# Performance work log

Measured on AMD Instinct MI355X. Metric: run time of the kernel, lower is better.

Reference implementation:

```python
import jax, jax.numpy as jnp
import numpy as np

EPS = 1e-12  # tf.math.l2_normalize epsilon

def l2norm(x):
    # tf.math.l2_normalize: x * rsqrt(max(sum(x^2), eps)) along last axis
    sq = jnp.sum(x * x, axis=-1, keepdims=True)
    return x * jax.lax.rsqrt(jnp.maximum(sq, EPS))

def setup_inputs() -> dict:
    key = jax.random.key(0)
    ks = jax.random.split(key, 10)
    B, L, D = 2, 512, 256
    OD = 256
    return {
        "queries": jax.random.normal(ks[0], (B, L, D), jnp.float32),
        "keys": jax.random.normal(ks[1], (B, L, D), jnp.float32),
        "values": jax.random.normal(ks[2], (B, L, D), jnp.float32),
        "relative_encoding_lookup": jax.random.normal(ks[3], (B, L, L, OD), jnp.float32),
        "edge_type_embedding": jax.random.normal(ks[4], (B, L, L, OD), jnp.float32),
        "Wq": jax.random.normal(ks[5], (D, OD), jnp.float32) * 0.05,
        "bq": jnp.zeros((OD,), jnp.float32),
        "Wk": jax.random.normal(ks[6], (D, OD), jnp.float32) * 0.05,
        "bk": jnp.zeros((OD,), jnp.float32),
        "Wv": jax.random.normal(ks[7], (D, OD), jnp.float32) * 0.05,
        "bv": jnp.zeros((OD,), jnp.float32),
    }

def reference(queries, keys, values, relative_encoding_lookup, edge_type_embedding,
              Wq, bq, Wk, bk, Wv, bv):
    d = queries.shape[-1]  # NOTE: original uses the INPUT dim (pre-projection) for scaling
    q = l2norm(jnp.matmul(queries, Wq) + bq)   # [B,L,OD]
    k = l2norm(jnp.matmul(keys, Wk) + bk)      # [B,L,OD]
    v = l2norm(jnp.matmul(values, Wv) + bv)    # [B,L,OD]
    scores_qk = jnp.einsum('bld,bmd->blm', q, k) * 0.4
    # Original broadcasts q to [B,L,L,OD] then multiply+reduce; expressed here as a
    # batched contraction (same math, no [B,L,L,OD] query broadcast materialized).
    # NOTE: the original computes scores_position (*0.2) but then overwrites it:
    #   scores = scores_ + scores_position; scores = scores_ + scores_edge_embedding
    # so scores_position is dead code and does NOT affect the output.
    scores_edge = jnp.einsum('bld,blmd->blm', q, edge_type_embedding) * 0.6
    inv_sqrt_d = jax.lax.rsqrt(jnp.float32(d))
    scores = (scores_qk + scores_edge) * inv_sqrt_d
    return scores, v, q
```

## Files before the change

kernel.cpp:

```cpp
#include <hip/hip_runtime.h>

#define SEQ_L 512
#define DIM 256

typedef float f4 __attribute__((ext_vector_type(4)));

__global__ __launch_bounds__(256) void proj_norm3_kernel(
    const float* __restrict__ Xq, const float* __restrict__ Wq,
    const float* __restrict__ bq, float* __restrict__ oq,
    const float* __restrict__ Xk, const float* __restrict__ Wk,
    const float* __restrict__ bk, float* __restrict__ ok,
    const float* __restrict__ Xv, const float* __restrict__ Wv,
    const float* __restrict__ bv, float* __restrict__ ov)
{
    const float* X; const float* W; const float* bias; float* out;
    if (blockIdx.y == 0)      { X = Xq; W = Wq; bias = bq; out = oq; }
    else if (blockIdx.y == 1) { X = Xk; W = Wk; bias = bk; out = ok; }
    else                      { X = Xv; W = Wv; bias = bv; out = ov; }

    const int ROWS = 8;
    __shared__ float xs[ROWS][DIM];
    __shared__ float red[ROWS][4];

    const int t  = threadIdx.x;
    const int r0 = blockIdx.x * ROWS;

    #pragma unroll
    for (int r = 0; r < ROWS; ++r)
        xs[r][t] = X[(size_t)(r0 + r) * DIM + t];
    __syncthreads();

    const float b = bias[t];
    float acc[ROWS];
    #pragma unroll
    for (int r = 0; r < ROWS; ++r) acc[r] = b;

    for (int d = 0; d < DIM; ++d) {
        const float wv = W[(size_t)d * DIM + t];
        #pragma unroll
        for (int r = 0; r < ROWS; ++r)
            acc[r] += xs[r][d] * wv;
    }

    const int lane = t & 63;
    const int wid  = t >> 6;

    #pragma unroll
    for (int r = 0; r < ROWS; ++r) {
        float ss = acc[r] * acc[r];
        #pragma unroll
        for (int off = 32; off >= 1; off >>= 1)
            ss += __shfl_down(ss, off, 64);
        if (lane == 0) red[r][wid] = ss;
    }
    __syncthreads();

    #pragma unroll
    for (int r = 0; r < ROWS; ++r) {
        const float s = red[r][0] + red[r][1] + red[r][2] + red[r][3];
        const float scale = rsqrtf(fmaxf(s, 1e-12f));
        out[(size_t)(r0 + r) * DIM + t] = acc[r] * scale;
    }
}

__global__ __launch_bounds__(256) void scores_kernel(
    const float* __restrict__ q, const float* __restrict__ k,
    const float* __restrict__ edge, float* __restrict__ out)
{
    const int bl    = blockIdx.x;
    const int b     = bl >> 9;
    const int lane  = threadIdx.x & 63;
    const int wave  = threadIdx.x >> 6;
    const int m_sub = lane & 7;
    const int d_sub = lane >> 3;

    const f4* q4 = (const f4*)(q + (size_t)bl * DIM);
    f4 qf[8];
    #pragma unroll
    for (int c = 0; c < 8; ++c) qf[c] = q4[c * 8 + d_sub];

    const f4* k4 = (const f4*)(k + (size_t)b * SEQ_L * DIM);
    const f4* e4 = (const f4*)(edge + (size_t)bl * SEQ_L * DIM);
    float* orow = out + (size_t)bl * SEQ_L;

    for (int m0 = wave * 8; m0 < SEQ_L; m0 += 32) {
        const size_t base = (size_t)(m0 + m_sub) * (DIM / 4) + d_sub;

        float ea = 0.f, eb = 0.f, ka = 0.f, kb = 0.f;
        #pragma unroll
        for (int c = 0; c < 8; ++c) {
            const f4 ef = __builtin_nontemporal_load(&e4[base + c * 8]);
            const f4 kf = k4[base + c * 8];
            ea += qf[c].x * ef.x + qf[c].y * ef.y;
            eb += qf[c].z * ef.z + qf[c].w * ef.w;
            ka += qf[c].x * kf.x + qf[c].y * kf.y;
            kb += qf[c].z * kf.z + qf[c].w * kf.w;
        }

        float s = 0.6f * (ea + eb) + 0.4f * (ka + kb);
        s += __shfl_xor(s, 8, 64);
        s += __shfl_xor(s, 16, 64);
        s += __shfl_xor(s, 32, 64);

        if (lane < 8) orow[m0 + lane] = s * 0.0625f;
    }
}

extern "C" void kernel_launch(void* const* d_in, const int* in_sizes, int n_in,
                              void* d_out, int out_size, void* d_ws, size_t ws_size,
                              hipStream_t stream) {
    const float* queries = (const float*)d_in[0];
    const float* keys    = (const float*)d_in[1];
    const float* values  = (const float*)d_in[2];
    const float* edge    = (const float*)d_in[4];
    const float* Wq = (const float*)d_in[5];
    const float* bq = (const float*)d_in[6];
    const float* Wk = (const float*)d_in[7];
    const float* bk = (const float*)d_in[8];
    const float* Wv = (const float*)d_in[9];
    const float* bv = (const float*)d_in[10];

    float* out = (float*)d_out;

    const int B = in_sizes[0] / (SEQ_L * DIM);
    const size_t scores_sz = (size_t)B * SEQ_L * SEQ_L;
    const size_t qkv_sz    = (size_t)B * SEQ_L * DIM;

    float* v_out = out + scores_sz;
    float* q_out = out + scores_sz + qkv_sz;
    float* k_ws  = (float*)d_ws;

    const int rows = B * SEQ_L;

    dim3 pgrid(rows / 8, 3);
    proj_norm3_kernel<<<pgrid, 256, 0, stream>>>(
        queries, Wq, bq, q_out,
        keys,    Wk, bk, k_ws,
        values,  Wv, bv, v_out);

    scores_kernel<<<rows, 256, 0, stream>>>(q_out, k_ws, edge, out);
}
```

Before: 144.9 us.

## Split QK and edge score computation into separate kernels with K reuse

Separates the fused scores kernel into a QK kernel that processes four query rows per block, reusing each loaded K tile across them, and an edge kernel that streams the large edge tensor with two m-rows in flight per iteration over a 2D grid. The edge kernel reads back the QK partial scores from the output and adds the scaled edge contribution. This cuts K reloads and raises memory-level parallelism on the dominant edge stream, at the cost of an extra kernel launch and an extra read and write of the scores array.

```diff
diff --git a/kernel.cpp b/kernel.cpp
--- a/kernel.cpp
+++ b/kernel.cpp
@@ -63,46 +63,102 @@
     }
 }
 
-__global__ __launch_bounds__(256) void scores_kernel(
+__global__ __launch_bounds__(256) void qk4_kernel(
     const float* __restrict__ q, const float* __restrict__ k,
-    const float* __restrict__ edge, float* __restrict__ out)
+    float* __restrict__ out)
 {
-    const int bl    = blockIdx.x;
-    const int b     = bl >> 9;
+    const int l0    = blockIdx.x * 4;
+    const int b     = l0 >> 9;
     const int lane  = threadIdx.x & 63;
     const int wave  = threadIdx.x >> 6;
     const int m_sub = lane & 7;
     const int d_sub = lane >> 3;
 
+    f4 qf[4][8];
+    #pragma unroll
+    for (int r = 0; r < 4; ++r) {
+        const f4* q4 = (const f4*)(q + (size_t)(l0 + r) * DIM);
+        #pragma unroll
+        for (int c = 0; c < 8; ++c) qf[r][c] = q4[c * 8 + d_sub];
+    }
+
+    const f4* k4 = (const f4*)(k + (size_t)b * SEQ_L * DIM);
+
+    for (int m0 = wave * 8; m0 < SEQ_L; m0 += 32) {
+        const size_t base = (size_t)(m0 + m_sub) * (DIM / 4) + d_sub;
+        f4 kf[8];
+        #pragma unroll
+        for (int c = 0; c < 8; ++c) kf[c] = k4[base + c * 8];
+
+        #pragma unroll
+        for (int r = 0; r < 4; ++r) {
+            float sa = 0.f, sb = 0.f;
+            #pragma unroll
+            for (int c = 0; c < 8; ++c) {
+                sa += qf[r][c].x * kf[c].x + qf[r][c].y * kf[c].y;
+                sb += qf[r][c].z * kf[c].z + qf[r][c].w * kf[c].w;
+            }
+            float s = sa + sb;
+            s += __shfl_xor(s, 8, 64);
+            s += __shfl_xor(s, 16, 64);
+            s += __shfl_xor(s, 32, 64);
+            if (lane < 8)
+                out[(size_t)(l0 + r) * SEQ_L + m0 + lane] = s * 0.025f;
+        }
+    }
+}
+
+__global__ __launch_bounds__(256) void edge_kernel(
+    const float* __restrict__ q, const float* __restrict__ edge,
+    float* __restrict__ out)
+{
+    const int bl    = blockIdx.x;
+    const int lane  = threadIdx.x & 63;
+    const int wave  = threadIdx.x >> 6;
+    const int m_sub = lane & 7;
+    const int d_sub = lane >> 3;
+
     const f4* q4 = (const f4*)(q + (size_t)bl * DIM);
     f4 qf[8];
     #pragma unroll
     for (int c = 0; c < 8; ++c) qf[c] = q4[c * 8 + d_sub];
 
-    const f4* k4 = (const f4*)(k + (size_t)b * SEQ_L * DIM);
     const f4* e4 = (const f4*)(edge + (size_t)bl * SEQ_L * DIM);
     float* orow = out + (size_t)bl * SEQ_L;
 
-    for (int m0 = wave * 8; m0 < SEQ_L; m0 += 32) {
-        const size_t base = (size_t)(m0 + m_sub) * (DIM / 4) + d_sub;
-
-        float ea = 0.f, eb = 0.f, ka = 0.f, kb = 0.f;
+    const int mbase = blockIdx.y * 256;
+    for (int m0 = mbase + wave * 8; m0 < mbase + 256; m0 += 64) {
+        const int m1 = m0 + 32;
+        const size_t ba0 = (size_t)(m0 + m_sub) * (DIM / 4) + d_sub;
+        const size_t ba1 = (size_t)(m1 + m_sub) * (DIM / 4) + d_sub;
+
+        f4 e0[8], e1[8];
         #pragma unroll
         for (int c = 0; c < 8; ++c) {
-            const f4 ef = __builtin_nontemporal_load(&e4[base + c * 8]);
-            const f4 kf = k4[base + c * 8];
-            ea += qf[c].x * ef.x + qf[c].y * ef.y;
-            eb += qf[c].z * ef.z + qf[c].w * ef.w;
-            ka += qf[c].x * kf.x + qf[c].y * kf.y;
-            kb += qf[c].z * kf.z + qf[c].w * kf.w;
-        }
-
-        float s = 0.6f * (ea + eb) + 0.4f * (ka + kb);
-        s += __shfl_xor(s, 8, 64);
-        s += __shfl_xor(s, 16, 64);
-        s += __shfl_xor(s, 32, 64);
-
-        if (lane < 8) orow[m0 + lane] = s * 0.0625f;
+            e0[c] = __builtin_nontemporal_load(&e4[ba0 + c * 8]);
+            e1[c] = __builtin_nontemporal_load(&e4[ba1 + c * 8]);
+        }
+
+        float base0 = 0.f, base1 = 0.f;
+        if (lane < 8) { base0 = orow[m0 + lane]; base1 = orow[m1 + lane]; }
+
+        float sa0 = 0.f, sb0 = 0.f, sa1 = 0.f, sb1 = 0.f;
+        #pragma unroll
+        for (int c = 0; c < 8; ++c) {
+            sa0 += qf[c].x * e0[c].x + qf[c].y * e0[c].y;
+            sb0 += qf[c].z * e0[c].z + qf[c].w * e0[c].w;
+            sa1 += qf[c].x * e1[c].x + qf[c].y * e1[c].y;
+            sb1 += qf[c].z * e1[c].z + qf[c].w * e1[c].w;
+        }
+        float s0 = sa0 + sb0, s1 = sa1 + sb1;
+        s0 += __shfl_xor(s0, 8, 64);  s1 += __shfl_xor(s1, 8, 64);
+        s0 += __shfl_xor(s0, 16, 64); s1 += __shfl_xor(s1, 16, 64);
+        s0 += __shfl_xor(s0, 32, 64); s1 += __shfl_xor(s1, 32, 64);
+
+        if (lane < 8) {
+            orow[m0 + lane] = fmaf(s0, 0.0375f, base0);
+            orow[m1 + lane] = fmaf(s1, 0.0375f, base1);
+        }
     }
 }
 
@@ -138,5 +194,8 @@
         keys,    Wk, bk, k_ws,
         values,  Wv, bv, v_out);
 
-    scores_kernel<<<rows, 256, 0, stream>>>(q_out, k_ws, edge, out);
-}
+    qk4_kernel<<<rows / 4, 256, 0, stream>>>(q_out, k_ws, out);
+
+    dim3 egrid(rows, 2);
+    edge_kernel<<<egrid, 256, 0, stream>>>(q_out, edge, out);
+}
```

Result: faster. 127.3 us (-12.1%).
